# Optimization experiments

Hardware: AMD Instinct MI355X
Metric: run time of the kernel (lower is better)

Reference implementation:

```python
import jax, jax.numpy as jnp
import numpy as np

B, N, OBS, ACT, H = 262144, 3, 30, 5, 64
IN = OBS + ACT  # 35
NEG_SLOPE_ATT = 0.2   # PyG GATConv default
NEG_SLOPE_MLP = 0.01
LN_EPS = 1e-5


def setup_inputs() -> dict:
    key = jax.random.key(0)
    ks = jax.random.split(key, 24)
    p = lambda k, shape, s=0.1: jax.random.normal(k, shape, jnp.float32) * s
    return {
        "obs": jax.random.normal(ks[0], (B, N * OBS), jnp.float32),
        "action": jax.random.normal(ks[1], (B, N * ACT), jnp.float32),
        "adj_matrix": jax.random.randint(ks[2], (B, N, N), 0, 2, jnp.int32),
        # GAT layer 1 (in=35 -> out=64, 1 head)
        "W1": p(ks[3], (IN, H)), "a1s": p(ks[4], (H,)), "a1d": p(ks[5], (H,)), "b1": jnp.zeros((H,), jnp.float32),
        # GAT layer 2 (in=64 -> out=64, 1 head)
        "W2": p(ks[6], (H, H)), "a2s": p(ks[7], (H,)), "a2d": p(ks[8], (H,)), "b2": jnp.zeros((H,), jnp.float32),
        # output_net: Linear(192,256)+LN, Linear(256,128)+LN, Linear(128,1)
        "Wo1": p(ks[9], (N * H, 256)), "bo1": jnp.zeros((256,), jnp.float32),
        "g1": jnp.ones((256,), jnp.float32), "be1": jnp.zeros((256,), jnp.float32),
        "Wo2": p(ks[10], (256, 128)), "bo2": jnp.zeros((128,), jnp.float32),
        "g2": jnp.ones((128,), jnp.float32), "be2": jnp.zeros((128,), jnp.float32),
        "Wo3": p(ks[11], (128, 1)), "bo3": jnp.zeros((1,), jnp.float32),
    }


def _gat(x, W, a_s, a_d, b, count):
    # x: [B,N,Din], count[b,i,j] = multiplicity of edge j->i (adj^T + self loop)
    z = jnp.einsum('bnd,de->bne', x, W)                      # [B,N,H]
    s_src = jnp.einsum('bnd,d->bn', z, a_s)                  # score contrib of source j
    s_dst = jnp.einsum('bnd,d->bn', z, a_d)                  # score contrib of target i
    e = jax.nn.leaky_relu(s_src[:, None, :] + s_dst[:, :, None], NEG_SLOPE_ATT)  # e[b,i,j]
    cnt = count.astype(z.dtype)
    m = jnp.max(jnp.where(count > 0, e, -jnp.inf), axis=-1, keepdims=True)  # self-loop guarantees finite
    p = cnt * jnp.exp(e - m)                                 # multiplicity-weighted softmax numerator
    alpha = p / jnp.sum(p, axis=-1, keepdims=True)           # [B,N,N]
    return jnp.einsum('bij,bjd->bid', alpha, z) + b


def _ln(x, g, be):
    mu = jnp.mean(x, axis=-1, keepdims=True)
    v = jnp.mean(jnp.square(x - mu), axis=-1, keepdims=True)
    return (x - mu) * jax.lax.rsqrt(v + LN_EPS) * g + be


def reference(obs, action, adj_matrix, W1, a1s, a1d, b1, W2, a2s, a2d, b2,
              Wo1, bo1, g1, be1, Wo2, bo2, g2, be2, Wo3, bo3):
    Bsz = obs.shape[0]
    x = jnp.concatenate([obs.reshape(Bsz, N, OBS), action.reshape(Bsz, N, ACT)], axis=-1)  # [B,N,35]
    # edge multiplicity: adj[b,s,t] means edge s->t; plus one self-loop per node
    count = jnp.swapaxes(adj_matrix, 1, 2) + jnp.eye(N, dtype=adj_matrix.dtype)  # count[b,i,j]
    h = jax.nn.elu(_gat(x, W1, a1s, a1d, b1, count))
    h = _gat(h, W2, a2s, a2d, b2, count)
    h = h.reshape(Bsz, N * H)
    h = jax.nn.leaky_relu(_ln(h @ Wo1 + bo1, g1, be1), NEG_SLOPE_MLP)
    h = jax.nn.leaky_relu(_ln(h @ Wo2 + bo2, g2, be2), NEG_SLOPE_MLP)
    return h @ Wo3 + bo3  # [B,1]
```

## Files before the change

### kernel.cpp

```cpp
#include <hip/hip_runtime.h>
#include <hip/hip_bf16.h>
#include <stdint.h>

#define B_TOT 262144

typedef __attribute__((ext_vector_type(8))) short bf8;
typedef __attribute__((ext_vector_type(16))) float f32x16;

__device__ __forceinline__ float bf2f(uint32_t u)   { return __uint_as_float(u << 16); }
__device__ __forceinline__ float bfhi2f(uint32_t u) { return __uint_as_float(u & 0xffff0000u); }
__device__ __forceinline__ uint32_t f2bf(float x) {
  uint32_t u = __float_as_uint(x);
  return (u + 0x7fffu + ((u >> 16) & 1u)) >> 16;
}
__device__ __forceinline__ uint32_t pkbf(float lo, float hi) {
  union { __hip_bfloat162 b; uint32_t u; } c;
  c.b = __float22bfloat162_rn(make_float2(lo, hi));
  return c.u;
}
__device__ __forceinline__ bf8 mkfrag(uint32_t w0, uint32_t w1, uint32_t w2, uint32_t w3) {
  union { uint32_t u[4]; bf8 v; } c;
  c.u[0] = w0; c.u[1] = w1; c.u[2] = w2; c.u[3] = w3;
  return c.v;
}

__global__ __launch_bounds__(256) void prep_kernel(
    const int* __restrict__ adj,
    const float* __restrict__ W1, const float* __restrict__ a1s, const float* __restrict__ a1d,
    const float* __restrict__ W2, const float* __restrict__ a2s, const float* __restrict__ a2d,
    const float* __restrict__ Wo1, const float* __restrict__ Wo2,
    uint32_t* __restrict__ cntp, uint16_t* __restrict__ W1F, uint16_t* __restrict__ W2F,
    uint16_t* __restrict__ Wo1F, uint16_t* __restrict__ Wo2F, float* __restrict__ wvec)
{
  const int gid = blockIdx.x * 256 + threadIdx.x;
  if (gid < B_TOT) {
    uint32_t cpv = 0;
    const int* ap = adj + (size_t)gid * 9;
    #pragma unroll
    for (int i = 0; i < 3; ++i)
      #pragma unroll
      for (int j = 0; j < 3; ++j) {
        uint32_t c = (uint32_t)ap[j * 3 + i] + (i == j ? 1u : 0u);
        cpv |= c << (2 * (3 * i + j));
      }
    cntp[gid] = cpv;
  }
  const int e = gid & 7, li = (gid >> 3) & 63;
  const int kfrag = 8 * (e >> 2) + 4 * (li >> 5) + (e & 3);
  if (gid < 3072) {
    const int f = gid >> 9, t = f & 1, ks = f >> 1;
    const int k = ks * 16 + kfrag, row = t * 32 + (li & 31);
    W1F[gid] = (uint16_t)f2bf(k < 35 ? W1[k * 64 + row] : 0.f);
  }
  if (gid < 4096) {
    const int f = gid >> 9, t = f & 1, ks = f >> 1;
    const int k = ks * 16 + kfrag, row = t * 32 + (li & 31);
    W2F[gid] = (uint16_t)f2bf(W2[k * 64 + row]);
  }
  if (gid < 49152) {
    const int rr = gid >> 9, t = rr & 7, ks = rr >> 3;
    const int k = ks * 16 + kfrag, col = t * 32 + (li & 31);
    Wo1F[gid] = (uint16_t)f2bf(Wo1[k * 256 + col]);
  }
  if (gid < 32768) {
    const int rr = gid >> 9, t = rr & 3, ks = rr >> 2;
    const int k = ks * 16 + kfrag, col = t * 32 + (li & 31);
    Wo2F[gid] = (uint16_t)f2bf(Wo2[k * 128 + col]);
  }
  if (gid < 224) {
    if (gid < 48) {
      float s = 0.f; if (gid < 35) for (int d = 0; d < 64; ++d) s += W1[gid * 64 + d] * a1s[d];
      wvec[gid] = s;
    } else if (gid < 96) {
      const int k = gid - 48; float s = 0.f;
      if (k < 35) for (int d = 0; d < 64; ++d) s += W1[k * 64 + d] * a1d[d];
      wvec[64 + k] = s;
    } else if (gid < 160) {
      const int k = gid - 96; float s = 0.f;
      for (int d = 0; d < 64; ++d) s += W2[k * 64 + d] * a2s[d];
      wvec[128 + k] = s;
    } else {
      const int k = gid - 160; float s = 0.f;
      for (int d = 0; d < 64; ++d) s += W2[k * 64 + d] * a2d[d];
      wvec[192 + k] = s;
    }
  }
}

template<bool DO_ELU, bool NS>
__device__ __forceinline__ void attention(const f32x16 (&az)[3][2],
    const float (&ss)[3], const float (&sd)[3], uint32_t cp, int hi,
    const float* __restrict__ bvec, const float* __restrict__ nxs, const float* __restrict__ nxd,
    uint32_t (&Ph)[3][16], float (&ss2)[3], float (&sd2)[3])
{
  float al[3][3];
  #pragma unroll
  for (int i = 0; i < 3; ++i) {
    float ev[3]; float mx = -1e30f;
    #pragma unroll
    for (int j = 0; j < 3; ++j) {
      float s = ss[j] + sd[i];
      s = fmaxf(s, 0.2f * s);
      ev[j] = s;
      int c = (cp >> (2 * (3 * i + j))) & 3;
      mx = fmaxf(mx, c ? s : -1e30f);
    }
    float sum = 0.f;
    #pragma unroll
    for (int j = 0; j < 3; ++j) {
      int c = (cp >> (2 * (3 * i + j))) & 3;
      float p = (float)c * __expf(ev[j] - mx);
      al[i][j] = p; sum += p;
    }
    float inv = 1.0f / sum;
    #pragma unroll
    for (int j = 0; j < 3; ++j) al[i][j] *= inv;
  }
  #pragma unroll
  for (int t = 0; t < 2; ++t) {
    float bv[16], nsv[16], ndv[16];
    #pragma unroll
    for (int rq = 0; rq < 4; ++rq) {
      float4 b4 = *reinterpret_cast<const float4*>(bvec + t * 32 + rq * 8 + hi * 4);
      bv[4 * rq + 0] = b4.x; bv[4 * rq + 1] = b4.y; bv[4 * rq + 2] = b4.z; bv[4 * rq + 3] = b4.w;
      if (NS) {
        float4 s4 = *reinterpret_cast<const float4*>(nxs + t * 32 + rq * 8 + hi * 4);
        float4 d4 = *reinterpret_cast<const float4*>(nxd + t * 32 + rq * 8 + hi * 4);
        nsv[4 * rq + 0] = s4.x; nsv[4 * rq + 1] = s4.y; nsv[4 * rq + 2] = s4.z; nsv[4 * rq + 3] = s4.w;
        ndv[4 * rq + 0] = d4.x; ndv[4 * rq + 1] = d4.y; ndv[4 * rq + 2] = d4.z; ndv[4 * rq + 3] = d4.w;
      }
    }
    #pragma unroll
    for (int i = 0; i < 3; ++i) {
      float hv[16];
      #pragma unroll
      for (int r = 0; r < 16; ++r) {
        float v = bv[r];
        v = fmaf(al[i][0], az[0][t][r], v);
        v = fmaf(al[i][1], az[1][t][r], v);
        v = fmaf(al[i][2], az[2][t][r], v);
        if (DO_ELU) v = v > 0.f ? v : (__expf(v) - 1.f);
        if (NS) { ss2[i] = fmaf(v, nsv[r], ss2[i]); sd2[i] = fmaf(v, ndv[r], sd2[i]); }
        hv[r] = v;
      }
      #pragma unroll
      for (int p = 0; p < 8; ++p) Ph[i][t * 8 + p] = pkbf(hv[2 * p], hv[2 * p + 1]);
    }
  }
}

__global__ __launch_bounds__(256, 2) void fused_kernel(
    const float* __restrict__ obs, const float* __restrict__ act,
    const uint32_t* __restrict__ cntp,
    const uint16_t* __restrict__ W1F, const uint16_t* __restrict__ W2F,
    const float* __restrict__ b1, const float* __restrict__ b2,
    const uint16_t* __restrict__ Wo1F, const float* __restrict__ bo1,
    const float* __restrict__ g1, const float* __restrict__ be1,
    const uint16_t* __restrict__ Wo2F, const float* __restrict__ bo2,
    const float* __restrict__ g2, const float* __restrict__ be2,
    const float* __restrict__ Wo3, const float* __restrict__ bo3,
    const float* __restrict__ wvec, float* __restrict__ out)
{
  __shared__ __align__(16) uint16_t Wo2s[32768];
  const int tid = threadIdx.x;
  {
    uint4* d3 = (uint4*)Wo2s; const uint4* s3 = (const uint4*)Wo2F;
    #pragma unroll
    for (int i = 0; i < 16; ++i) d3[tid + 256 * i] = s3[tid + 256 * i];
  }

  const int l = tid & 63, hi = l >> 5, col = l & 31;
  const int wid = blockIdx.x * 4 + (tid >> 6);
  const int e = wid * 32 + col;
  const uint32_t cp = cntp[e];
  const float* obs_e = obs + (size_t)e * 90;
  const float* act_e = act + (size_t)e * 15;

  f32x16 az[3][2];
  #pragma unroll
  for (int n = 0; n < 3; ++n)
    #pragma unroll
    for (int t = 0; t < 2; ++t)
      #pragma unroll
      for (int r = 0; r < 16; ++r) az[n][t][r] = 0.f;
  float ss1[3] = {0, 0, 0}, sd1[3] = {0, 0, 0};

  #pragma unroll
  for (int ks = 0; ks < 3; ++ks) {
    bf8 xh[3], xl[3];
    #pragma unroll
    for (int n = 0; n < 3; ++n) {
      const float* on = obs_e + n * 30;
      float xv[8];
      #pragma unroll
      for (int r2 = 0; r2 < 2; ++r2) {
        if (ks == 2 && r2 == 1) { xv[4] = xv[5] = xv[6] = xv[7] = 0.f; continue; }
        const int kb = ks * 16 + r2 * 8 + hi * 4;
        #pragma unroll
        for (int j = 0; j < 4; ++j) {
          const int k = kb + j;
          float v = 0.f;
          if (k < 30) v = on[k];
          else if (k < 35) v = act_e[n * 5 + k - 30];
          xv[r2 * 4 + j] = v;
        }
        float4 s4 = *reinterpret_cast<const float4*>(wvec + kb);
        float4 d4 = *reinterpret_cast<const float4*>(wvec + 64 + kb);
        ss1[n] = fmaf(xv[r2 * 4 + 0], s4.x, ss1[n]); sd1[n] = fmaf(xv[r2 * 4 + 0], d4.x, sd1[n]);
        ss1[n] = fmaf(xv[r2 * 4 + 1], s4.y, ss1[n]); sd1[n] = fmaf(xv[r2 * 4 + 1], d4.y, sd1[n]);
        ss1[n] = fmaf(xv[r2 * 4 + 2], s4.z, ss1[n]); sd1[n] = fmaf(xv[r2 * 4 + 2], d4.z, sd1[n]);
        ss1[n] = fmaf(xv[r2 * 4 + 3], s4.w, ss1[n]); sd1[n] = fmaf(xv[r2 * 4 + 3], d4.w, sd1[n]);
      }
      uint32_t hw[4], lw[4];
      #pragma unroll
      for (int p = 0; p < 4; ++p) {
        hw[p] = pkbf(xv[2 * p], xv[2 * p + 1]);
        float ra = xv[2 * p]     - bf2f(hw[p]);
        float rb = xv[2 * p + 1] - bfhi2f(hw[p]);
        lw[p] = (__float_as_uint(ra) >> 16) | (__float_as_uint(rb) & 0xffff0000u);
      }
      xh[n] = mkfrag(hw[0], hw[1], hw[2], hw[3]);
      xl[n] = mkfrag(lw[0], lw[1], lw[2], lw[3]);
    }
    #pragma unroll
    for (int t = 0; t < 2; ++t) {
      bf8 a = *reinterpret_cast<const bf8*>(W1F + (size_t)((ks * 2 + t) * 64 + l) * 8);
      #pragma unroll
      for (int n = 0; n < 3; ++n) {
        az[n][t] = __builtin_amdgcn_mfma_f32_32x32x16_bf16(a, xh[n], az[n][t], 0, 0, 0);
        az[n][t] = __builtin_amdgcn_mfma_f32_32x32x16_bf16(a, xl[n], az[n][t], 0, 0, 0);
      }
    }
  }
  #pragma unroll
  for (int n = 0; n < 3; ++n) {
    ss1[n] += __shfl_xor(ss1[n], 32);
    sd1[n] += __shfl_xor(sd1[n], 32);
  }

  uint32_t Ph1[3][16];
  float ss2[3] = {0, 0, 0}, sd2[3] = {0, 0, 0};
  attention<true, true>(az, ss1, sd1, cp, hi, b1, wvec + 128, wvec + 192, Ph1, ss2, sd2);
  #pragma unroll
  for (int n = 0; n < 3; ++n) {
    ss2[n] += __shfl_xor(ss2[n], 32);
    sd2[n] += __shfl_xor(sd2[n], 32);
  }

  f32x16 a2[3][2];
  #pragma unroll
  for (int n = 0; n < 3; ++n)
    #pragma unroll
    for (int t = 0; t < 2; ++t)
      #pragma unroll
      for (int r = 0; r < 16; ++r) a2[n][t][r] = 0.f;
  #pragma unroll
  for (int ks = 0; ks < 4; ++ks) {
    #pragma unroll
    for (int t = 0; t < 2; ++t) {
      bf8 a = *reinterpret_cast<const bf8*>(W2F + (size_t)((ks * 2 + t) * 64 + l) * 8);
      #pragma unroll
      for (int n = 0; n < 3; ++n) {
        bf8 br_ = mkfrag(Ph1[n][4 * ks], Ph1[n][4 * ks + 1], Ph1[n][4 * ks + 2], Ph1[n][4 * ks + 3]);
        a2[n][t] = __builtin_amdgcn_mfma_f32_32x32x16_bf16(a, br_, a2[n][t], 0, 0, 0);
      }
    }
  }

  uint32_t Ph2[3][16];
  float du1[3], du2[3];
  attention<false, false>(a2, ss2, sd2, cp, hi, b2, nullptr, nullptr, Ph2, du1, du2);

  __syncthreads();

  float sm = 0.f, sq = 0.f;
  uint32_t y[64];
  #pragma unroll
  for (int half = 0; half < 2; ++half) {
    f32x16 acc[4];
    #pragma unroll
    for (int t = 0; t < 4; ++t)
      #pragma unroll
      for (int rq = 0; rq < 4; ++rq) {
        float4 b4 = *reinterpret_cast<const float4*>(bo1 + (half * 4 + t) * 32 + rq * 8 + hi * 4);
        acc[t][4 * rq + 0] = b4.x; acc[t][4 * rq + 1] = b4.y;
        acc[t][4 * rq + 2] = b4.z; acc[t][4 * rq + 3] = b4.w;
      }
    #pragma unroll
    for (int ks = 0; ks < 12; ++ks) {
      const int n = ks >> 2, q0 = 4 * (ks & 3);
      bf8 br_ = mkfrag(Ph2[n][q0], Ph2[n][q0 + 1], Ph2[n][q0 + 2], Ph2[n][q0 + 3]);
      #pragma unroll
      for (int t = 0; t < 4; ++t) {
        bf8 a = *reinterpret_cast<const bf8*>(Wo1F + (size_t)((ks * 8 + half * 4 + t) * 64 + l) * 8);
        acc[t] = __builtin_amdgcn_mfma_f32_32x32x16_bf16(a, br_, acc[t], 0, 0, 0);
      }
    }
    #pragma unroll
    for (int t = 0; t < 4; ++t) {
      #pragma unroll
      for (int r = 0; r < 16; ++r) { const float v = acc[t][r]; sm += v; sq = fmaf(v, v, sq); }
      #pragma unroll
      for (int p = 0; p < 8; ++p)
        y[(half * 4 + t) * 8 + p] = pkbf(acc[t][2 * p], acc[t][2 * p + 1]);
    }
  }
  sm += __shfl_xor(sm, 32); sq += __shfl_xor(sq, 32);
  float mu = sm * (1.f / 256.f);
  float rr = rsqrtf(sq * (1.f / 256.f) - mu * mu + 1e-5f);
  #pragma unroll
  for (int tg = 0; tg < 8; ++tg)
    #pragma unroll
    for (int rq = 0; rq < 4; ++rq) {
      float4 gg = *reinterpret_cast<const float4*>(g1 + tg * 32 + rq * 8 + hi * 4);
      float4 bb = *reinterpret_cast<const float4*>(be1 + tg * 32 + rq * 8 + hi * 4);
      const int w0 = tg * 8 + rq * 2;
      float v0 = (bf2f(y[w0]) - mu) * rr * gg.x + bb.x;        v0 = fmaxf(v0, 0.01f * v0);
      float v1 = (bfhi2f(y[w0]) - mu) * rr * gg.y + bb.y;      v1 = fmaxf(v1, 0.01f * v1);
      y[w0] = pkbf(v0, v1);
      float v2 = (bf2f(y[w0 + 1]) - mu) * rr * gg.z + bb.z;    v2 = fmaxf(v2, 0.01f * v2);
      float v3 = (bfhi2f(y[w0 + 1]) - mu) * rr * gg.w + bb.w;  v3 = fmaxf(v3, 0.01f * v3);
      y[w0 + 1] = pkbf(v2, v3);
    }

  f32x16 acc2[4];
  #pragma unroll
  for (int t = 0; t < 4; ++t)
    #pragma unroll
    for (int rq = 0; rq < 4; ++rq) {
      float4 b4 = *reinterpret_cast<const float4*>(bo2 + t * 32 + rq * 8 + hi * 4);
      acc2[t][4 * rq + 0] = b4.x; acc2[t][4 * rq + 1] = b4.y;
      acc2[t][4 * rq + 2] = b4.z; acc2[t][4 * rq + 3] = b4.w;
    }
  #pragma unroll
  for (int ks = 0; ks < 16; ++ks) {
    bf8 br_ = mkfrag(y[4 * ks], y[4 * ks + 1], y[4 * ks + 2], y[4 * ks + 3]);
    #pragma unroll
    for (int t = 0; t < 4; ++t) {
      bf8 a = *reinterpret_cast<const bf8*>(&Wo2s[(ks * 4 + t) * 512 + l * 8]);
      acc2[t] = __builtin_amdgcn_mfma_f32_32x32x16_bf16(a, br_, acc2[t], 0, 0, 0);
    }
  }
  sm = 0.f; sq = 0.f;
  #pragma unroll
  for (int t = 0; t < 4; ++t)
    #pragma unroll
    for (int r = 0; r < 16; ++r) { const float v = acc2[t][r]; sm += v; sq = fmaf(v, v, sq); }
  sm += __shfl_xor(sm, 32); sq += __shfl_xor(sq, 32);
  mu = sm * (1.f / 128.f);
  rr = rsqrtf(sq * (1.f / 128.f) - mu * mu + 1e-5f);
  float acy = 0.f;
  #pragma unroll
  for (int t = 0; t < 4; ++t)
    #pragma unroll
    for (int rq = 0; rq < 4; ++rq) {
      float4 gg = *reinterpret_cast<const float4*>(g2 + t * 32 + rq * 8 + hi * 4);
      float4 bb = *reinterpret_cast<const float4*>(be2 + t * 32 + rq * 8 + hi * 4);
      float4 ww = *reinterpret_cast<const float4*>(Wo3 + t * 32 + rq * 8 + hi * 4);
      float v;
      v = (acc2[t][4 * rq + 0] - mu) * rr * gg.x + bb.x; acy = fmaf(fmaxf(v, 0.01f * v), ww.x, acy);
      v = (acc2[t][4 * rq + 1] - mu) * rr * gg.y + bb.y; acy = fmaf(fmaxf(v, 0.01f * v), ww.y, acy);
      v = (acc2[t][4 * rq + 2] - mu) * rr * gg.z + bb.z; acy = fmaf(fmaxf(v, 0.01f * v), ww.z, acy);
      v = (acc2[t][4 * rq + 3] - mu) * rr * gg.w + bb.w; acy = fmaf(fmaxf(v, 0.01f * v), ww.w, acy);
    }
  acy += __shfl_xor(acy, 32);
  if (hi == 0) out[e] = acy + bo3[0];
}

extern "C" void kernel_launch(void* const* d_in, const int* in_sizes, int n_in,
                              void* d_out, int out_size, void* d_ws, size_t ws_size,
                              hipStream_t stream) {
  const float* obs  = (const float*)d_in[0];
  const float* actn = (const float*)d_in[1];
  const int*   adj  = (const int*)d_in[2];
  const float* W1   = (const float*)d_in[3];
  const float* a1s  = (const float*)d_in[4];
  const float* a1d  = (const float*)d_in[5];
  const float* b1   = (const float*)d_in[6];
  const float* W2   = (const float*)d_in[7];
  const float* a2s  = (const float*)d_in[8];
  const float* a2d  = (const float*)d_in[9];
  const float* b2   = (const float*)d_in[10];
  const float* Wo1  = (const float*)d_in[11];
  const float* bo1  = (const float*)d_in[12];
  const float* g1   = (const float*)d_in[13];
  const float* be1  = (const float*)d_in[14];
  const float* Wo2  = (const float*)d_in[15];
  const float* bo2  = (const float*)d_in[16];
  const float* g2   = (const float*)d_in[17];
  const float* be2  = (const float*)d_in[18];
  const float* Wo3  = (const float*)d_in[19];
  const float* bo3  = (const float*)d_in[20];

  char* ws = (char*)d_ws;
  uint32_t* cntp = (uint32_t*)ws;
  uint16_t* W1F  = (uint16_t*)(ws + 1048576);
  uint16_t* W2F  = (uint16_t*)(ws + 1048576 + 8192);
  uint16_t* Wo1F = (uint16_t*)(ws + 1048576 + 16384);
  uint16_t* Wo2F = (uint16_t*)(ws + 1048576 + 114688);
  float*    wvec = (float*)(ws + 1048576 + 180224);
  float* outp = (float*)d_out;

  prep_kernel<<<1024, 256, 0, stream>>>(adj, W1, a1s, a1d, W2, a2s, a2d, Wo1, Wo2,
                                        cntp, W1F, W2F, Wo1F, Wo2F, wvec);
  fused_kernel<<<2048, 256, 0, stream>>>(obs, actn, cntp, W1F, W2F, b1, b2,
                                         Wo1F, bo1, g1, be1, Wo2F, bo2, g2, be2,
                                         Wo3, bo3, wvec, outp);
}
```

Before: 122.6 us.

## Spill node activations to per-thread LDS and raise occupancy to three blocks

Per-thread GAT activations (Ph1/Ph2) move from registers into a per-thread strided LDS buffer. The LDS copy of Wo2 is dropped, so Wo2 is now read from global memory or cache. Several loops are set to unroll 1 and the Wo1 halves are split into separate blocks to cut register pressure, and launch bounds go from 2 to 3 blocks per CU. This trades extra LDS traffic and global weight loads for higher occupancy and latency hiding.

```diff
diff --git a/kernel.cpp b/kernel.cpp
--- a/kernel.cpp
+++ b/kernel.cpp
@@ -91,7 +91,7 @@
 __device__ __forceinline__ void attention(const f32x16 (&az)[3][2],
     const float (&ss)[3], const float (&sd)[3], uint32_t cp, int hi,
     const float* __restrict__ bvec, const float* __restrict__ nxs, const float* __restrict__ nxd,
-    uint32_t (&Ph)[3][16], float (&ss2)[3], float (&sd2)[3])
+    uint32_t* phc, float (&ss2)[3], float (&sd2)[3])
 {
   float al[3][3];
   #pragma unroll
@@ -144,12 +144,13 @@
         hv[r] = v;
       }
       #pragma unroll
-      for (int p = 0; p < 8; ++p) Ph[i][t * 8 + p] = pkbf(hv[2 * p], hv[2 * p + 1]);
-    }
-  }
-}
-
-__global__ __launch_bounds__(256, 2) void fused_kernel(
+      for (int p = 0; p < 8; ++p)
+        phc[(i * 16 + t * 8 + p) << 8] = pkbf(hv[2 * p], hv[2 * p + 1]);
+    }
+  }
+}
+
+__global__ __launch_bounds__(256, 3) void fused_kernel(
     const float* __restrict__ obs, const float* __restrict__ act,
     const uint32_t* __restrict__ cntp,
     const uint16_t* __restrict__ W1F, const uint16_t* __restrict__ W2F,
@@ -161,13 +162,9 @@
     const float* __restrict__ Wo3, const float* __restrict__ bo3,
     const float* __restrict__ wvec, float* __restrict__ out)
 {
-  __shared__ __align__(16) uint16_t Wo2s[32768];
+  __shared__ uint32_t ph[48 * 256];
   const int tid = threadIdx.x;
-  {
-    uint4* d3 = (uint4*)Wo2s; const uint4* s3 = (const uint4*)Wo2F;
-    #pragma unroll
-    for (int i = 0; i < 16; ++i) d3[tid + 256 * i] = s3[tid + 256 * i];
-  }
+  uint32_t* phc = ph + tid;
 
   const int l = tid & 63, hi = l >> 5, col = l & 31;
   const int wid = blockIdx.x * 4 + (tid >> 6);
@@ -185,23 +182,21 @@
       for (int r = 0; r < 16; ++r) az[n][t][r] = 0.f;
   float ss1[3] = {0, 0, 0}, sd1[3] = {0, 0, 0};
 
-  #pragma unroll
+  #pragma unroll 1
   for (int ks = 0; ks < 3; ++ks) {
-    bf8 xh[3], xl[3];
     #pragma unroll
     for (int n = 0; n < 3; ++n) {
       const float* on = obs_e + n * 30;
       float xv[8];
       #pragma unroll
       for (int r2 = 0; r2 < 2; ++r2) {
-        if (ks == 2 && r2 == 1) { xv[4] = xv[5] = xv[6] = xv[7] = 0.f; continue; }
         const int kb = ks * 16 + r2 * 8 + hi * 4;
         #pragma unroll
         for (int j = 0; j < 4; ++j) {
           const int k = kb + j;
           float v = 0.f;
           if (k < 30) v = on[k];
-          else if (k < 35) v = act_e[n * 5 + k - 30];
+          else if (k < 35) v = act_e[n * 5 + (k - 30)];
           xv[r2 * 4 + j] = v;
         }
         float4 s4 = *reinterpret_cast<const float4*>(wvec + kb);
@@ -219,16 +214,13 @@
         float rb = xv[2 * p + 1] - bfhi2f(hw[p]);
         lw[p] = (__float_as_uint(ra) >> 16) | (__float_as_uint(rb) & 0xffff0000u);
       }
-      xh[n] = mkfrag(hw[0], hw[1], hw[2], hw[3]);
-      xl[n] = mkfrag(lw[0], lw[1], lw[2], lw[3]);
-    }
-    #pragma unroll
-    for (int t = 0; t < 2; ++t) {
-      bf8 a = *reinterpret_cast<const bf8*>(W1F + (size_t)((ks * 2 + t) * 64 + l) * 8);
-      #pragma unroll
-      for (int n = 0; n < 3; ++n) {
-        az[n][t] = __builtin_amdgcn_mfma_f32_32x32x16_bf16(a, xh[n], az[n][t], 0, 0, 0);
-        az[n][t] = __builtin_amdgcn_mfma_f32_32x32x16_bf16(a, xl[n], az[n][t], 0, 0, 0);
+      bf8 xh = mkfrag(hw[0], hw[1], hw[2], hw[3]);
+      bf8 xl = mkfrag(lw[0], lw[1], lw[2], lw[3]);
+      #pragma unroll
+      for (int t = 0; t < 2; ++t) {
+        bf8 a = *reinterpret_cast<const bf8*>(W1F + (size_t)(ks * 2 + t) * 512 + l * 8);
+        az[n][t] = __builtin_amdgcn_mfma_f32_32x32x16_bf16(a, xh, az[n][t], 0, 0, 0);
+        az[n][t] = __builtin_amdgcn_mfma_f32_32x32x16_bf16(a, xl, az[n][t], 0, 0, 0);
       }
     }
   }
@@ -238,9 +230,8 @@
     sd1[n] += __shfl_xor(sd1[n], 32);
   }
 
-  uint32_t Ph1[3][16];
   float ss2[3] = {0, 0, 0}, sd2[3] = {0, 0, 0};
-  attention<true, true>(az, ss1, sd1, cp, hi, b1, wvec + 128, wvec + 192, Ph1, ss2, sd2);
+  attention<true, true>(az, ss1, sd1, cp, hi, b1, wvec + 128, wvec + 192, phc, ss2, sd2);
   #pragma unroll
   for (int n = 0; n < 3; ++n) {
     ss2[n] += __shfl_xor(ss2[n], 32);
@@ -254,45 +245,46 @@
     for (int t = 0; t < 2; ++t)
       #pragma unroll
       for (int r = 0; r < 16; ++r) a2[n][t][r] = 0.f;
-  #pragma unroll
+  #pragma unroll 1
   for (int ks = 0; ks < 4; ++ks) {
+    bf8 br[3];
+    #pragma unroll
+    for (int n = 0; n < 3; ++n) {
+      const int wb = (n * 16 + ks * 4) << 8;
+      br[n] = mkfrag(phc[wb], phc[wb + 256], phc[wb + 512], phc[wb + 768]);
+    }
     #pragma unroll
     for (int t = 0; t < 2; ++t) {
-      bf8 a = *reinterpret_cast<const bf8*>(W2F + (size_t)((ks * 2 + t) * 64 + l) * 8);
-      #pragma unroll
-      for (int n = 0; n < 3; ++n) {
-        bf8 br_ = mkfrag(Ph1[n][4 * ks], Ph1[n][4 * ks + 1], Ph1[n][4 * ks + 2], Ph1[n][4 * ks + 3]);
-        a2[n][t] = __builtin_amdgcn_mfma_f32_32x32x16_bf16(a, br_, a2[n][t], 0, 0, 0);
-      }
-    }
-  }
-
-  uint32_t Ph2[3][16];
+      bf8 a = *reinterpret_cast<const bf8*>(W2F + (size_t)(ks * 2 + t) * 512 + l * 8);
+      #pragma unroll
+      for (int n = 0; n < 3; ++n)
+        a2[n][t] = __builtin_amdgcn_mfma_f32_32x32x16_bf16(a, br[n], a2[n][t], 0, 0, 0);
+    }
+  }
+
   float du1[3], du2[3];
-  attention<false, false>(a2, ss2, sd2, cp, hi, b2, nullptr, nullptr, Ph2, du1, du2);
-
-  __syncthreads();
+  attention<false, false>(a2, ss2, sd2, cp, hi, b2, nullptr, nullptr, phc, du1, du2);
 
   float sm = 0.f, sq = 0.f;
   uint32_t y[64];
-  #pragma unroll
-  for (int half = 0; half < 2; ++half) {
+  {
     f32x16 acc[4];
     #pragma unroll
     for (int t = 0; t < 4; ++t)
       #pragma unroll
       for (int rq = 0; rq < 4; ++rq) {
-        float4 b4 = *reinterpret_cast<const float4*>(bo1 + (half * 4 + t) * 32 + rq * 8 + hi * 4);
+        float4 b4 = *reinterpret_cast<const float4*>(bo1 + t * 32 + rq * 8 + hi * 4);
         acc[t][4 * rq + 0] = b4.x; acc[t][4 * rq + 1] = b4.y;
         acc[t][4 * rq + 2] = b4.z; acc[t][4 * rq + 3] = b4.w;
       }
-    #pragma unroll
+    #pragma unroll 1
     for (int ks = 0; ks < 12; ++ks) {
-      const int n = ks >> 2, q0 = 4 * (ks & 3);
-      bf8 br_ = mkfrag(Ph2[n][q0], Ph2[n][q0 + 1], Ph2[n][q0 + 2], Ph2[n][q0 + 3]);
+      const int wb = ((ks >> 2) * 16 + (ks & 3) * 4) << 8;
+      bf8 br_ = mkfrag(phc[wb], phc[wb + 256], phc[wb + 512], phc[wb + 768]);
+      const uint16_t* wp = Wo1F + (size_t)(ks * 8) * 512 + l * 8;
       #pragma unroll
       for (int t = 0; t < 4; ++t) {
-        bf8 a = *reinterpret_cast<const bf8*>(Wo1F + (size_t)((ks * 8 + half * 4 + t) * 64 + l) * 8);
+        bf8 a = *reinterpret_cast<const bf8*>(wp + t * 512);
         acc[t] = __builtin_amdgcn_mfma_f32_32x32x16_bf16(a, br_, acc[t], 0, 0, 0);
       }
     }
@@ -301,8 +293,36 @@
       #pragma unroll
       for (int r = 0; r < 16; ++r) { const float v = acc[t][r]; sm += v; sq = fmaf(v, v, sq); }
       #pragma unroll
-      for (int p = 0; p < 8; ++p)
-        y[(half * 4 + t) * 8 + p] = pkbf(acc[t][2 * p], acc[t][2 * p + 1]);
+      for (int p = 0; p < 8; ++p) y[t * 8 + p] = pkbf(acc[t][2 * p], acc[t][2 * p + 1]);
+    }
+  }
+  {
+    f32x16 acc[4];
+    #pragma unroll
+    for (int t = 0; t < 4; ++t)
+      #pragma unroll
+      for (int rq = 0; rq < 4; ++rq) {
+        float4 b4 = *reinterpret_cast<const float4*>(bo1 + (4 + t) * 32 + rq * 8 + hi * 4);
+        acc[t][4 * rq + 0] = b4.x; acc[t][4 * rq + 1] = b4.y;
+        acc[t][4 * rq + 2] = b4.z; acc[t][4 * rq + 3] = b4.w;
+      }
+    #pragma unroll 1
+    for (int ks = 0; ks < 12; ++ks) {
+      const int wb = ((ks >> 2) * 16 + (ks & 3) * 4) << 8;
+      bf8 br_ = mkfrag(phc[wb], phc[wb + 256], phc[wb + 512], phc[wb + 768]);
+      const uint16_t* wp = Wo1F + (size_t)(ks * 8 + 4) * 512 + l * 8;
+      #pragma unroll
+      for (int t = 0; t < 4; ++t) {
+        bf8 a = *reinterpret_cast<const bf8*>(wp + t * 512);
+        acc[t] = __builtin_amdgcn_mfma_f32_32x32x16_bf16(a, br_, acc[t], 0, 0, 0);
+      }
+    }
+    #pragma unroll
+    for (int t = 0; t < 4; ++t) {
+      #pragma unroll
+      for (int r = 0; r < 16; ++r) { const float v = acc[t][r]; sm += v; sq = fmaf(v, v, sq); }
+      #pragma unroll
+      for (int p = 0; p < 8; ++p) y[32 + t * 8 + p] = pkbf(acc[t][2 * p], acc[t][2 * p + 1]);
     }
   }
   sm += __shfl_xor(sm, 32); sq += __shfl_xor(sq, 32);
@@ -337,7 +357,7 @@
     bf8 br_ = mkfrag(y[4 * ks], y[4 * ks + 1], y[4 * ks + 2], y[4 * ks + 3]);
     #pragma unroll
     for (int t = 0; t < 4; ++t) {
-      bf8 a = *reinterpret_cast<const bf8*>(&Wo2s[(ks * 4 + t) * 512 + l * 8]);
+      bf8 a = *reinterpret_cast<const bf8*>(Wo2F + (size_t)(ks * 4 + t) * 512 + l * 8);
       acc2[t] = __builtin_amdgcn_mfma_f32_32x32x16_bf16(a, br_, acc2[t], 0, 0, 0);
     }
   }
```

After: 256.6 us. 2.09x slower.

## Stage per-wave obs/action tiles in LDS with coalesced loads; read Wo2 from global

Applied to the files above, without the earlier changes.

Each wave now copies its 32 samples' obs and action rows into shared memory with contiguous 8-byte loads before layer 1, replacing strided per-lane global gathers. The shared buffer that used to hold Wo2 is repurposed for this, so Wo2 fragments are read directly from global memory (via cache) in the second MLP layer. The block-wide __syncthreads-dependent Wo2 preload is gone, but Wo2 reads now hit L1/L2 instead of LDS. Weight index expressions are also simplified.

```diff
diff --git a/kernel.cpp b/kernel.cpp
--- a/kernel.cpp
+++ b/kernel.cpp
@@ -161,20 +161,27 @@
     const float* __restrict__ Wo3, const float* __restrict__ bo3,
     const float* __restrict__ wvec, float* __restrict__ out)
 {
-  __shared__ __align__(16) uint16_t Wo2s[32768];
+  __shared__ float xs[4 * 3392];
   const int tid = threadIdx.x;
+  const int l = tid & 63, hi = l >> 5, col = l & 31;
+  const int w = tid >> 6;
+  const int wid = blockIdx.x * 4 + w;
+  const int e = wid * 32 + col;
+  float* xw = xs + w * 3392;
+
   {
-    uint4* d3 = (uint4*)Wo2s; const uint4* s3 = (const uint4*)Wo2F;
-    #pragma unroll
-    for (int i = 0; i < 16; ++i) d3[tid + 256 * i] = s3[tid + 256 * i];
-  }
-
-  const int l = tid & 63, hi = l >> 5, col = l & 31;
-  const int wid = blockIdx.x * 4 + (tid >> 6);
-  const int e = wid * 32 + col;
+    const uint2* __restrict__ og = (const uint2*)(obs + (size_t)(wid * 32) * 90);
+    const uint2* __restrict__ ag = (const uint2*)(act + (size_t)(wid * 32) * 15);
+    uint2* ow = (uint2*)xw;
+    #pragma unroll
+    for (int i = 0; i < 22; ++i) ow[l + 64 * i] = og[l + 64 * i];
+    if (l < 32) ow[1408 + l] = og[1408 + l];
+    uint2* aw = (uint2*)(xw + 2880);
+    #pragma unroll
+    for (int i = 0; i < 3; ++i) aw[l + 64 * i] = ag[l + 64 * i];
+    if (l < 48) aw[192 + l] = ag[192 + l];
+  }
   const uint32_t cp = cntp[e];
-  const float* obs_e = obs + (size_t)e * 90;
-  const float* act_e = act + (size_t)e * 15;
 
   f32x16 az[3][2];
   #pragma unroll
@@ -190,7 +197,6 @@
     bf8 xh[3], xl[3];
     #pragma unroll
     for (int n = 0; n < 3; ++n) {
-      const float* on = obs_e + n * 30;
       float xv[8];
       #pragma unroll
       for (int r2 = 0; r2 < 2; ++r2) {
@@ -199,9 +205,10 @@
         #pragma unroll
         for (int j = 0; j < 4; ++j) {
           const int k = kb + j;
-          float v = 0.f;
-          if (k < 30) v = on[k];
-          else if (k < 35) v = act_e[n * 5 + k - 30];
+          const int off = (k < 30) ? (col * 90 + n * 30 + k)
+                                   : (2880 + col * 15 + n * 5 + (k - 30));
+          float v = xw[off];
+          if (k >= 35) v = 0.f;
           xv[r2 * 4 + j] = v;
         }
         float4 s4 = *reinterpret_cast<const float4*>(wvec + kb);
@@ -224,7 +231,7 @@
     }
     #pragma unroll
     for (int t = 0; t < 2; ++t) {
-      bf8 a = *reinterpret_cast<const bf8*>(W1F + (size_t)((ks * 2 + t) * 64 + l) * 8);
+      bf8 a = *reinterpret_cast<const bf8*>(W1F + (size_t)(ks * 2 + t) * 512 + l * 8);
       #pragma unroll
       for (int n = 0; n < 3; ++n) {
         az[n][t] = __builtin_amdgcn_mfma_f32_32x32x16_bf16(a, xh[n], az[n][t], 0, 0, 0);
@@ -258,7 +265,7 @@
   for (int ks = 0; ks < 4; ++ks) {
     #pragma unroll
     for (int t = 0; t < 2; ++t) {
-      bf8 a = *reinterpret_cast<const bf8*>(W2F + (size_t)((ks * 2 + t) * 64 + l) * 8);
+      bf8 a = *reinterpret_cast<const bf8*>(W2F + (size_t)(ks * 2 + t) * 512 + l * 8);
       #pragma unroll
       for (int n = 0; n < 3; ++n) {
         bf8 br_ = mkfrag(Ph1[n][4 * ks], Ph1[n][4 * ks + 1], Ph1[n][4 * ks + 2], Ph1[n][4 * ks + 3]);
@@ -292,7 +299,7 @@
       bf8 br_ = mkfrag(Ph2[n][q0], Ph2[n][q0 + 1], Ph2[n][q0 + 2], Ph2[n][q0 + 3]);
       #pragma unroll
       for (int t = 0; t < 4; ++t) {
-        bf8 a = *reinterpret_cast<const bf8*>(Wo1F + (size_t)((ks * 8 + half * 4 + t) * 64 + l) * 8);
+        bf8 a = *reinterpret_cast<const bf8*>(Wo1F + (size_t)(ks * 8 + half * 4 + t) * 512 + l * 8);
         acc[t] = __builtin_amdgcn_mfma_f32_32x32x16_bf16(a, br_, acc[t], 0, 0, 0);
       }
     }
@@ -337,7 +344,7 @@
     bf8 br_ = mkfrag(y[4 * ks], y[4 * ks + 1], y[4 * ks + 2], y[4 * ks + 3]);
     #pragma unroll
     for (int t = 0; t < 4; ++t) {
-      bf8 a = *reinterpret_cast<const bf8*>(&Wo2s[(ks * 4 + t) * 512 + l * 8]);
+      bf8 a = *reinterpret_cast<const bf8*>(Wo2F + (size_t)(ks * 4 + t) * 512 + l * 8);
       acc2[t] = __builtin_amdgcn_mfma_f32_32x32x16_bf16(a, br_, acc2[t], 0, 0, 0);
     }
   }
```

Result: slower. 210.2 us (+71.5%).

## Split output MLP across warps by feature columns with LDS-staged activations

Applied to the files above, without the earlier changes.

Instead of each warp computing the full 256- and 128-wide output MLP for its own 32 elements, the block now stages layer-2 GAT activations for all 128 elements in shared memory. Each warp then computes a slice of output features for all four element groups, so every weight fragment is loaded once and reused across four MFMAs. Wo2 is now read from global memory instead of being preloaded into LDS. LayerNorm statistics and the final dot product are reduced across warps through shared memory. This cuts weight-fragment traffic per element and register pressure, at the cost of extra __syncthreads and LDS round trips.

```diff
diff --git a/kernel.cpp b/kernel.cpp
--- a/kernel.cpp
+++ b/kernel.cpp
@@ -87,13 +87,9 @@
   }
 }
 
-template<bool DO_ELU, bool NS>
-__device__ __forceinline__ void attention(const f32x16 (&az)[3][2],
-    const float (&ss)[3], const float (&sd)[3], uint32_t cp, int hi,
-    const float* __restrict__ bvec, const float* __restrict__ nxs, const float* __restrict__ nxd,
-    uint32_t (&Ph)[3][16], float (&ss2)[3], float (&sd2)[3])
+__device__ __forceinline__ void att_alpha(const float (&ss)[3], const float (&sd)[3],
+                                          uint32_t cp, float (&al)[3][3])
 {
-  float al[3][3];
   #pragma unroll
   for (int i = 0; i < 3; ++i) {
     float ev[3]; float mx = -1e30f;
@@ -116,19 +112,26 @@
     #pragma unroll
     for (int j = 0; j < 3; ++j) al[i][j] *= inv;
   }
+}
+
+__device__ __forceinline__ void attention1(const f32x16 (&az)[3][2],
+    const float (&ss)[3], const float (&sd)[3], uint32_t cp, int hi,
+    const float* __restrict__ bvec, const float* __restrict__ nxs, const float* __restrict__ nxd,
+    uint32_t (&Ph)[3][16], float (&ss2)[3], float (&sd2)[3])
+{
+  float al[3][3];
+  att_alpha(ss, sd, cp, al);
   #pragma unroll
   for (int t = 0; t < 2; ++t) {
     float bv[16], nsv[16], ndv[16];
     #pragma unroll
     for (int rq = 0; rq < 4; ++rq) {
       float4 b4 = *reinterpret_cast<const float4*>(bvec + t * 32 + rq * 8 + hi * 4);
+      float4 s4 = *reinterpret_cast<const float4*>(nxs + t * 32 + rq * 8 + hi * 4);
+      float4 d4 = *reinterpret_cast<const float4*>(nxd + t * 32 + rq * 8 + hi * 4);
       bv[4 * rq + 0] = b4.x; bv[4 * rq + 1] = b4.y; bv[4 * rq + 2] = b4.z; bv[4 * rq + 3] = b4.w;
-      if (NS) {
-        float4 s4 = *reinterpret_cast<const float4*>(nxs + t * 32 + rq * 8 + hi * 4);
-        float4 d4 = *reinterpret_cast<const float4*>(nxd + t * 32 + rq * 8 + hi * 4);
-        nsv[4 * rq + 0] = s4.x; nsv[4 * rq + 1] = s4.y; nsv[4 * rq + 2] = s4.z; nsv[4 * rq + 3] = s4.w;
-        ndv[4 * rq + 0] = d4.x; ndv[4 * rq + 1] = d4.y; ndv[4 * rq + 2] = d4.z; ndv[4 * rq + 3] = d4.w;
-      }
+      nsv[4 * rq + 0] = s4.x; nsv[4 * rq + 1] = s4.y; nsv[4 * rq + 2] = s4.z; nsv[4 * rq + 3] = s4.w;
+      ndv[4 * rq + 0] = d4.x; ndv[4 * rq + 1] = d4.y; ndv[4 * rq + 2] = d4.z; ndv[4 * rq + 3] = d4.w;
     }
     #pragma unroll
     for (int i = 0; i < 3; ++i) {
@@ -139,12 +142,44 @@
         v = fmaf(al[i][0], az[0][t][r], v);
         v = fmaf(al[i][1], az[1][t][r], v);
         v = fmaf(al[i][2], az[2][t][r], v);
-        if (DO_ELU) v = v > 0.f ? v : (__expf(v) - 1.f);
-        if (NS) { ss2[i] = fmaf(v, nsv[r], ss2[i]); sd2[i] = fmaf(v, ndv[r], sd2[i]); }
+        v = v > 0.f ? v : (__expf(v) - 1.f);
+        ss2[i] = fmaf(v, nsv[r], ss2[i]); sd2[i] = fmaf(v, ndv[r], sd2[i]);
         hv[r] = v;
       }
       #pragma unroll
       for (int p = 0; p < 8; ++p) Ph[i][t * 8 + p] = pkbf(hv[2 * p], hv[2 * p + 1]);
+    }
+  }
+}
+
+__device__ __forceinline__ void attention2(const f32x16 (&az)[3][2],
+    const float (&ss)[3], const float (&sd)[3], uint32_t cp, int hi,
+    const float* __restrict__ bvec, uint32_t* __restrict__ ldscol)
+{
+  float al[3][3];
+  att_alpha(ss, sd, cp, al);
+  #pragma unroll
+  for (int t = 0; t < 2; ++t) {
+    float bv[16];
+    #pragma unroll
+    for (int rq = 0; rq < 4; ++rq) {
+      float4 b4 = *reinterpret_cast<const float4*>(bvec + t * 32 + rq * 8 + hi * 4);
+      bv[4 * rq + 0] = b4.x; bv[4 * rq + 1] = b4.y; bv[4 * rq + 2] = b4.z; bv[4 * rq + 3] = b4.w;
+    }
+    #pragma unroll
+    for (int i = 0; i < 3; ++i) {
+      float hv[16];
+      #pragma unroll
+      for (int r = 0; r < 16; ++r) {
+        float v = bv[r];
+        v = fmaf(al[i][0], az[0][t][r], v);
+        v = fmaf(al[i][1], az[1][t][r], v);
+        v = fmaf(al[i][2], az[2][t][r], v);
+        hv[r] = v;
+      }
+      #pragma unroll
+      for (int p = 0; p < 8; ++p)
+        ldscol[(i * 16 + t * 8 + p) * 256] = pkbf(hv[2 * p], hv[2 * p + 1]);
     }
   }
 }
@@ -161,17 +196,12 @@
     const float* __restrict__ Wo3, const float* __restrict__ bo3,
     const float* __restrict__ wvec, float* __restrict__ out)
 {
-  __shared__ __align__(16) uint16_t Wo2s[32768];
+  __shared__ uint32_t buf[16384];
   const int tid = threadIdx.x;
-  {
-    uint4* d3 = (uint4*)Wo2s; const uint4* s3 = (const uint4*)Wo2F;
-    #pragma unroll
-    for (int i = 0; i < 16; ++i) d3[tid + 256 * i] = s3[tid + 256 * i];
-  }
-
   const int l = tid & 63, hi = l >> 5, col = l & 31;
-  const int wid = blockIdx.x * 4 + (tid >> 6);
-  const int e = wid * 32 + col;
+  const int w = tid >> 6;
+  const int eb = w * 32 + col;
+  const int e = blockIdx.x * 128 + eb;
   const uint32_t cp = cntp[e];
   const float* obs_e = obs + (size_t)e * 90;
   const float* act_e = act + (size_t)e * 15;
@@ -201,7 +231,7 @@
           const int k = kb + j;
           float v = 0.f;
           if (k < 30) v = on[k];
-          else if (k < 35) v = act_e[n * 5 + k - 30];
+          else if (k < 35) v = act_e[n * 5 + (k - 30)];
           xv[r2 * 4 + j] = v;
         }
         float4 s4 = *reinterpret_cast<const float4*>(wvec + kb);
@@ -224,7 +254,7 @@
     }
     #pragma unroll
     for (int t = 0; t < 2; ++t) {
-      bf8 a = *reinterpret_cast<const bf8*>(W1F + (size_t)((ks * 2 + t) * 64 + l) * 8);
+      bf8 a = *reinterpret_cast<const bf8*>(W1F + (size_t)(ks * 2 + t) * 512 + l * 8);
       #pragma unroll
       for (int n = 0; n < 3; ++n) {
         az[n][t] = __builtin_amdgcn_mfma_f32_32x32x16_bf16(a, xh[n], az[n][t], 0, 0, 0);
@@ -240,7 +270,7 @@
 
   uint32_t Ph1[3][16];
   float ss2[3] = {0, 0, 0}, sd2[3] = {0, 0, 0};
-  attention<true, true>(az, ss1, sd1, cp, hi, b1, wvec + 128, wvec + 192, Ph1, ss2, sd2);
+  attention1(az, ss1, sd1, cp, hi, b1, wvec + 128, wvec + 192, Ph1, ss2, sd2);
   #pragma unroll
   for (int n = 0; n < 3; ++n) {
     ss2[n] += __shfl_xor(ss2[n], 32);
@@ -258,7 +288,7 @@
   for (int ks = 0; ks < 4; ++ks) {
     #pragma unroll
     for (int t = 0; t < 2; ++t) {
-      bf8 a = *reinterpret_cast<const bf8*>(W2F + (size_t)((ks * 2 + t) * 64 + l) * 8);
+      bf8 a = *reinterpret_cast<const bf8*>(W2F + (size_t)(ks * 2 + t) * 512 + l * 8);
       #pragma unroll
       for (int n = 0; n < 3; ++n) {
         bf8 br_ = mkfrag(Ph1[n][4 * ks], Ph1[n][4 * ks + 1], Ph1[n][4 * ks + 2], Ph1[n][4 * ks + 3]);
@@ -267,104 +297,178 @@
     }
   }
 
-  uint32_t Ph2[3][16];
-  float du1[3], du2[3];
-  attention<false, false>(a2, ss2, sd2, cp, hi, b2, nullptr, nullptr, Ph2, du1, du2);
-
-  __syncthreads();
-
-  float sm = 0.f, sq = 0.f;
-  uint32_t y[64];
-  #pragma unroll
-  for (int half = 0; half < 2; ++half) {
-    f32x16 acc[4];
-    #pragma unroll
-    for (int t = 0; t < 4; ++t)
+  attention2(a2, ss2, sd2, cp, hi, b2, buf + (hi * 128 + eb));
+  __syncthreads();
+
+  const int fb1 = w * 64;
+  f32x16 acc[2][4];
+  #pragma unroll
+  for (int t = 0; t < 2; ++t)
+    #pragma unroll
+    for (int rq = 0; rq < 4; ++rq) {
+      float4 b4 = *reinterpret_cast<const float4*>(bo1 + fb1 + t * 32 + rq * 8 + hi * 4);
+      #pragma unroll
+      for (int eg = 0; eg < 4; ++eg) {
+        acc[t][eg][4 * rq + 0] = b4.x; acc[t][eg][4 * rq + 1] = b4.y;
+        acc[t][eg][4 * rq + 2] = b4.z; acc[t][eg][4 * rq + 3] = b4.w;
+      }
+    }
+  #pragma unroll
+  for (int ks = 0; ks < 12; ++ks) {
+    bf8 bfr[4];
+    #pragma unroll
+    for (int eg = 0; eg < 4; ++eg) {
+      const uint32_t* pc = buf + (hi * 128 + eg * 32 + col) + ks * 4 * 256;
+      bfr[eg] = mkfrag(pc[0], pc[256], pc[512], pc[768]);
+    }
+    #pragma unroll
+    for (int t = 0; t < 2; ++t) {
+      bf8 a = *reinterpret_cast<const bf8*>(Wo1F + (size_t)(ks * 8 + w * 2 + t) * 512 + l * 8);
+      #pragma unroll
+      for (int eg = 0; eg < 4; ++eg)
+        acc[t][eg] = __builtin_amdgcn_mfma_f32_32x32x16_bf16(a, bfr[eg], acc[t][eg], 0, 0, 0);
+    }
+  }
+  {
+    float psm[4], psq[4];
+    #pragma unroll
+    for (int eg = 0; eg < 4; ++eg) { psm[eg] = 0.f; psq[eg] = 0.f; }
+    #pragma unroll
+    for (int t = 0; t < 2; ++t)
+      #pragma unroll
+      for (int eg = 0; eg < 4; ++eg)
+        #pragma unroll
+        for (int r = 0; r < 16; ++r) {
+          const float v = acc[t][eg][r]; psm[eg] += v; psq[eg] = fmaf(v, v, psq[eg]);
+        }
+    float* part = (float*)buf + 12288;
+    #pragma unroll
+    for (int eg = 0; eg < 4; ++eg) {
+      psm[eg] += __shfl_xor(psm[eg], 32);
+      psq[eg] += __shfl_xor(psq[eg], 32);
+      if (hi == 0) {
+        part[w * 128 + eg * 32 + col] = psm[eg];
+        part[512 + w * 128 + eg * 32 + col] = psq[eg];
+      }
+    }
+  }
+  __syncthreads();
+  float mu1[4], rr1[4];
+  {
+    const float* part = (const float*)buf + 12288;
+    #pragma unroll
+    for (int eg = 0; eg < 4; ++eg) {
+      const int ei = eg * 32 + col;
+      float s = part[ei] + part[128 + ei] + part[256 + ei] + part[384 + ei];
+      float q = part[512 + ei] + part[640 + ei] + part[768 + ei] + part[896 + ei];
+      mu1[eg] = s * (1.f / 256.f);
+      rr1[eg] = rsqrtf(q * (1.f / 256.f) - mu1[eg] * mu1[eg] + 1e-5f);
+    }
+  }
+  __syncthreads();
+  #pragma unroll
+  for (int t = 0; t < 2; ++t)
+    #pragma unroll
+    for (int rq = 0; rq < 4; ++rq) {
+      float4 gg = *reinterpret_cast<const float4*>(g1 + fb1 + t * 32 + rq * 8 + hi * 4);
+      float4 bb = *reinterpret_cast<const float4*>(be1 + fb1 + t * 32 + rq * 8 + hi * 4);
+      #pragma unroll
+      for (int eg = 0; eg < 4; ++eg) {
+        float v0 = (acc[t][eg][4 * rq + 0] - mu1[eg]) * rr1[eg] * gg.x + bb.x; v0 = fmaxf(v0, 0.01f * v0);
+        float v1 = (acc[t][eg][4 * rq + 1] - mu1[eg]) * rr1[eg] * gg.y + bb.y; v1 = fmaxf(v1, 0.01f * v1);
+        float v2 = (acc[t][eg][4 * rq + 2] - mu1[eg]) * rr1[eg] * gg.z + bb.z; v2 = fmaxf(v2, 0.01f * v2);
+        float v3 = (acc[t][eg][4 * rq + 3] - mu1[eg]) * rr1[eg] * gg.w + bb.w; v3 = fmaxf(v3, 0.01f * v3);
+        const int c = hi * 128 + eg * 32 + col;
+        buf[(w * 16 + t * 8 + rq * 2 + 0) * 256 + c] = pkbf(v0, v1);
+        buf[(w * 16 + t * 8 + rq * 2 + 1) * 256 + c] = pkbf(v2, v3);
+      }
+    }
+  __syncthreads();
+
+  const int fb2 = w * 32;
+  f32x16 acc2[4];
+  #pragma unroll
+  for (int rq = 0; rq < 4; ++rq) {
+    float4 b4 = *reinterpret_cast<const float4*>(bo2 + fb2 + rq * 8 + hi * 4);
+    #pragma unroll
+    for (int eg = 0; eg < 4; ++eg) {
+      acc2[eg][4 * rq + 0] = b4.x; acc2[eg][4 * rq + 1] = b4.y;
+      acc2[eg][4 * rq + 2] = b4.z; acc2[eg][4 * rq + 3] = b4.w;
+    }
+  }
+  #pragma unroll
+  for (int ks = 0; ks < 16; ++ks) {
+    bf8 bfr[4];
+    #pragma unroll
+    for (int eg = 0; eg < 4; ++eg) {
+      const uint32_t* pc = buf + (hi * 128 + eg * 32 + col) + ks * 4 * 256;
+      bfr[eg] = mkfrag(pc[0], pc[256], pc[512], pc[768]);
+    }
+    bf8 a = *reinterpret_cast<const bf8*>(Wo2F + (size_t)(ks * 4 + w) * 512 + l * 8);
+    #pragma unroll
+    for (int eg = 0; eg < 4; ++eg)
+      acc2[eg] = __builtin_amdgcn_mfma_f32_32x32x16_bf16(a, bfr[eg], acc2[eg], 0, 0, 0);
+  }
+  __syncthreads();
+  {
+    float psm[4], psq[4];
+    #pragma unroll
+    for (int eg = 0; eg < 4; ++eg) { psm[eg] = 0.f; psq[eg] = 0.f; }
+    #pragma unroll
+    for (int eg = 0; eg < 4; ++eg)
+      #pragma unroll
+      for (int r = 0; r < 16; ++r) {
+        const float v = acc2[eg][r]; psm[eg] += v; psq[eg] = fmaf(v, v, psq[eg]);
+      }
+    float* part = (float*)buf;
+    #pragma unroll
+    for (int eg = 0; eg < 4; ++eg) {
+      psm[eg] += __shfl_xor(psm[eg], 32);
+      psq[eg] += __shfl_xor(psq[eg], 32);
+      if (hi == 0) {
+        part[w * 128 + eg * 32 + col] = psm[eg];
+        part[512 + w * 128 + eg * 32 + col] = psq[eg];
+      }
+    }
+  }
+  __syncthreads();
+  {
+    const float* part = (const float*)buf;
+    float* p3 = (float*)buf + 1024;
+    float dot[4];
+    #pragma unroll
+    for (int eg = 0; eg < 4; ++eg) {
+      const int ei = eg * 32 + col;
+      float s = part[ei] + part[128 + ei] + part[256 + ei] + part[384 + ei];
+      float q = part[512 + ei] + part[640 + ei] + part[768 + ei] + part[896 + ei];
+      const float mu = s * (1.f / 128.f);
+      const float rr = rsqrtf(q * (1.f / 128.f) - mu * mu + 1e-5f);
+      float d = 0.f;
       #pragma unroll
       for (int rq = 0; rq < 4; ++rq) {
-        float4 b4 = *reinterpret_cast<const float4*>(bo1 + (half * 4 + t) * 32 + rq * 8 + hi * 4);
-        acc[t][4 * rq + 0] = b4.x; acc[t][4 * rq + 1] = b4.y;
-        acc[t][4 * rq + 2] = b4.z; acc[t][4 * rq + 3] = b4.w;
-      }
-    #pragma unroll
-    for (int ks = 0; ks < 12; ++ks) {
-      const int n = ks >> 2, q0 = 4 * (ks & 3);
-      bf8 br_ = mkfrag(Ph2[n][q0], Ph2[n][q0 + 1], Ph2[n][q0 + 2], Ph2[n][q0 + 3]);
-      #pragma unroll
-      for (int t = 0; t < 4; ++t) {
-        bf8 a = *reinterpret_cast<const bf8*>(Wo1F + (size_t)((ks * 8 + half * 4 + t) * 64 + l) * 8);
-        acc[t] = __builtin_amdgcn_mfma_f32_32x32x16_bf16(a, br_, acc[t], 0, 0, 0);
-      }
-    }
-    #pragma unroll
-    for (int t = 0; t < 4; ++t) {
-      #pragma unroll
-      for (int r = 0; r < 16; ++r) { const float v = acc[t][r]; sm += v; sq = fmaf(v, v, sq); }
-      #pragma unroll
-      for (int p = 0; p < 8; ++p)
-        y[(half * 4 + t) * 8 + p] = pkbf(acc[t][2 * p], acc[t][2 * p + 1]);
-    }
-  }
-  sm += __shfl_xor(sm, 32); sq += __shfl_xor(sq, 32);
-  float mu = sm * (1.f / 256.f);
-  float rr = rsqrtf(sq * (1.f / 256.f) - mu * mu + 1e-5f);
-  #pragma unroll
-  for (int tg = 0; tg < 8; ++tg)
-    #pragma unroll
-    for (int rq = 0; rq < 4; ++rq) {
-      float4 gg = *reinterpret_cast<const float4*>(g1 + tg * 32 + rq * 8 + hi * 4);
-      float4 bb = *reinterpret_cast<const float4*>(be1 + tg * 32 + rq * 8 + hi * 4);
-      const int w0 = tg * 8 + rq * 2;
-      float v0 = (bf2f(y[w0]) - mu) * rr * gg.x + bb.x;        v0 = fmaxf(v0, 0.01f * v0);
-      float v1 = (bfhi2f(y[w0]) - mu) * rr * gg.y + bb.y;      v1 = fmaxf(v1, 0.01f * v1);
-      y[w0] = pkbf(v0, v1);
-      float v2 = (bf2f(y[w0 + 1]) - mu) * rr * gg.z + bb.z;    v2 = fmaxf(v2, 0.01f * v2);
-      float v3 = (bfhi2f(y[w0 + 1]) - mu) * rr * gg.w + bb.w;  v3 = fmaxf(v3, 0.01f * v3);
-      y[w0 + 1] = pkbf(v2, v3);
-    }
-
-  f32x16 acc2[4];
-  #pragma unroll
-  for (int t = 0; t < 4; ++t)
-    #pragma unroll
-    for (int rq = 0; rq < 4; ++rq) {
-      float4 b4 = *reinterpret_cast<const float4*>(bo2 + t * 32 + rq * 8 + hi * 4);
-      acc2[t][4 * rq + 0] = b4.x; acc2[t][4 * rq + 1] = b4.y;
-      acc2[t][4 * rq + 2] = b4.z; acc2[t][4 * rq + 3] = b4.w;
-    }
-  #pragma unroll
-  for (int ks = 0; ks < 16; ++ks) {
-    bf8 br_ = mkfrag(y[4 * ks], y[4 * ks + 1], y[4 * ks + 2], y[4 * ks + 3]);
-    #pragma unroll
-    for (int t = 0; t < 4; ++t) {
-      bf8 a = *reinterpret_cast<const bf8*>(&Wo2s[(ks * 4 + t) * 512 + l * 8]);
-      acc2[t] = __builtin_amdgcn_mfma_f32_32x32x16_bf16(a, br_, acc2[t], 0, 0, 0);
-    }
-  }
-  sm = 0.f; sq = 0.f;
-  #pragma unroll
-  for (int t = 0; t < 4; ++t)
-    #pragma unroll
-    for (int r = 0; r < 16; ++r) { const float v = acc2[t][r]; sm += v; sq = fmaf(v, v, sq); }
-  sm += __shfl_xor(sm, 32); sq += __shfl_xor(sq, 32);
-  mu = sm * (1.f / 128.f);
-  rr = rsqrtf(sq * (1.f / 128.f) - mu * mu + 1e-5f);
-  float acy = 0.f;
-  #pragma unroll
-  for (int t = 0; t < 4; ++t)
-    #pragma unroll
-    for (int rq = 0; rq < 4; ++rq) {
-      float4 gg = *reinterpret_cast<const float4*>(g2 + t * 32 + rq * 8 + hi * 4);
-      float4 bb = *reinterpret_cast<const float4*>(be2 + t * 32 + rq * 8 + hi * 4);
-      float4 ww = *reinterpret_cast<const float4*>(Wo3 + t * 32 + rq * 8 + hi * 4);
-      float v;
-      v = (acc2[t][4 * rq + 0] - mu) * rr * gg.x + bb.x; acy = fmaf(fmaxf(v, 0.01f * v), ww.x, acy);
-      v = (acc2[t][4 * rq + 1] - mu) * rr * gg.y + bb.y; acy = fmaf(fmaxf(v, 0.01f * v), ww.y, acy);
-      v = (acc2[t][4 * rq + 2] - mu) * rr * gg.z + bb.z; acy = fmaf(fmaxf(v, 0.01f * v), ww.z, acy);
-      v = (acc2[t][4 * rq + 3] - mu) * rr * gg.w + bb.w; acy = fmaf(fmaxf(v, 0.01f * v), ww.w, acy);
-    }
-  acy += __shfl_xor(acy, 32);
-  if (hi == 0) out[e] = acy + bo3[0];
+        float4 gg = *reinterpret_cast<const float4*>(g2 + fb2 + rq * 8 + hi * 4);
+        float4 bb = *reinterpret_cast<const float4*>(be2 + fb2 + rq * 8 + hi * 4);
+        float4 ww = *reinterpret_cast<const float4*>(Wo3 + fb2 + rq * 8 + hi * 4);
+        float v;
+        v = (acc2[eg][4 * rq + 0] - mu) * rr * gg.x + bb.x; d = fmaf(fmaxf(v, 0.01f * v), ww.x, d);
+        v = (acc2[eg][4 * rq + 1] - mu) * rr * gg.y + bb.y; d = fmaf(fmaxf(v, 0.01f * v), ww.y, d);
+        v = (acc2[eg][4 * rq + 2] - mu) * rr * gg.z + bb.z; d = fmaf(fmaxf(v, 0.01f * v), ww.z, d);
+        v = (acc2[eg][4 * rq + 3] - mu) * rr * gg.w + bb.w; d = fmaf(fmaxf(v, 0.01f * v), ww.w, d);
+      }
+      dot[eg] = d;
+    }
+    #pragma unroll
+    for (int eg = 0; eg < 4; ++eg) {
+      dot[eg] += __shfl_xor(dot[eg], 32);
+      if (hi == 0) p3[w * 128 + eg * 32 + col] = dot[eg];
+    }
+  }
+  __syncthreads();
+  if (tid < 128) {
+    const float* p3 = (const float*)buf + 1024;
+    out[blockIdx.x * 128 + tid] =
+        p3[tid] + p3[128 + tid] + p3[256 + tid] + p3[384 + tid] + bo3[0];
+  }
 }
 
 extern "C" void kernel_launch(void* const* d_in, const int* in_sizes, int n_in,
```

Result: faster. 118.1 us (-3.6%).
